# Kernel tuning notes

Hardware: AMD Instinct MI355X
Metric: run time of the kernel (lower is better)

The kernel has to match this reference:

```python
import jax, jax.numpy as jnp
import numpy as np

# canonical 3x3 lattice offsets, (dy,dx) pairs in row-major kernel order (mmcv offset layout)
CANON = jnp.array([[-1,-1],[-1,0],[-1,1],[0,-1],[0,0],[0,1],[1,-1],[1,0],[1,1]], dtype=jnp.float32)  # (9,2)
BASE_DILATION = 1.0

def conv3x3(x, w, b):
    # x: (B,Cin,H,W), w: (Cout,Cin,3,3), stride 1, pad 1
    y = jax.lax.conv_general_dilated(x, w, window_strides=(1, 1), padding=((1, 1), (1, 1)),
                                     dimension_numbers=('NCHW', 'OIHW', 'NCHW'))
    return y + b[None, :, None, None]

def _bilinear_sample(img, ys, xs):
    # img: (Cg,H,W); ys,xs: (9,H,W) float sample coords. Zero outside bounds (per-corner).
    Cg, Hn, Wn = img.shape
    y0 = jnp.floor(ys); x0 = jnp.floor(xs)
    wy = ys - y0; wx = xs - x0
    y0i = y0.astype(jnp.int32); x0i = x0.astype(jnp.int32)
    flat = img.reshape(Cg, Hn * Wn)
    def corner(yi, xi, w):
        valid = (yi >= 0) & (yi < Hn) & (xi >= 0) & (xi < Wn)
        idx = jnp.clip(yi, 0, Hn - 1) * Wn + jnp.clip(xi, 0, Wn - 1)
        v = jnp.take(flat, idx.reshape(-1), axis=1).reshape((Cg,) + yi.shape)
        return v * (w * valid.astype(img.dtype))[None]
    return (corner(y0i, x0i, (1 - wy) * (1 - wx)) + corner(y0i, x0i + 1, (1 - wy) * wx)
            + corner(y0i + 1, x0i, wy * (1 - wx)) + corner(y0i + 1, x0i + 1, wy * wx))  # (Cg,9,H,W)

def setup_inputs() -> dict:
    key = jax.random.key(0)
    ks = jax.random.split(key, 7)
    B, C, H, W = 4, 256, 64, 64
    O, dg = 256, 1
    x = jax.random.normal(ks[0], (B, C, H, W), dtype=jnp.float32)
    weight = jax.random.normal(ks[1], (O, C, 3, 3), dtype=jnp.float32) * (2.0 / (C * 9)) ** 0.5
    bias = jnp.zeros((O,), dtype=jnp.float32)
    w_scale = jax.random.normal(ks[2], (dg, C, 3, 3), dtype=jnp.float32) * 0.01
    b_scale = jnp.full((dg,), 0.5, dtype=jnp.float32)
    w_mask = jax.random.normal(ks[3], (dg * 9, C, 3, 3), dtype=jnp.float32) * 0.01
    b_mask = jnp.zeros((dg * 9,), dtype=jnp.float32)
    return {"x": x, "weight": weight, "bias": bias, "w_scale": w_scale,
            "b_scale": b_scale, "w_mask": w_mask, "b_mask": b_mask}

def reference(x, weight, bias, w_scale, b_scale, w_mask, b_mask):
    B, C, H, W = x.shape
    dg = w_scale.shape[0]
    O = weight.shape[0]
    Cg = C // dg
    # radial scale s(x) >= 0 (use_zero_dilation=False): (B,dg,H,W)
    scale = jax.nn.relu(conv3x3(x, w_scale, b_scale)) * BASE_DILATION
    # modulation mask: (B,dg,9,H,W)
    mask = jax.nn.sigmoid(conv3x3(x, w_mask, b_mask)).reshape(B, dg, 9, H, W)
    # learned offset = scale * canonical lattice: (B,dg,9,2,H,W)
    off = scale[:, :, None, None, :, :] * CANON[None, None, :, :, None, None]
    # sampling coords: p0 (out pos * stride - pad) + kernel offset * dilation(=1) + learned offset
    base_y = jnp.arange(H, dtype=x.dtype)[None, None, None, :, None] - 1.0  # pad=1
    base_x = jnp.arange(W, dtype=x.dtype)[None, None, None, None, :] - 1.0
    ys = base_y + CANON[:, 0][None, None, :, None, None] + off[:, :, :, 0]  # (B,dg,9,H,W)
    xs = base_x + CANON[:, 1][None, None, :, None, None] + off[:, :, :, 1]
    xg = x.reshape(B, dg, Cg, H, W)
    sampled = jax.vmap(jax.vmap(_bilinear_sample))(xg, ys, xs)  # (B,dg,Cg,9,H,W)
    val = (sampled * mask[:, :, None]).reshape(B, C, 9, H, W)
    out = jnp.einsum('bckhw,ock->bohw', val, weight.reshape(O, C, 9))
    return out + bias[None, :, None, None]
```

## Files before the change

### kernel.cpp

```cpp
#include <hip/hip_runtime.h>
#include <stdint.h>

#define B_ 4
#define C_ 256
#define H_ 64
#define W_ 64
#define O_ 256
#define K_ 2304
#define HW 4096
#define NPIX 16384

typedef unsigned short u16;
typedef __attribute__((ext_vector_type(8))) short bf16x8;
typedef __attribute__((ext_vector_type(4))) float f32x4;

__device__ __forceinline__ u16 f2bf(float f) {
    union { float f; uint32_t u; } v; v.f = f;
    uint32_t u = v.u;
    return (u16)((u + 0x7FFFu + ((u >> 16) & 1u)) >> 16);
}
__device__ __forceinline__ float bf2f(u16 u) {
    union { uint32_t u; float f; } v; v.u = ((uint32_t)u) << 16;
    return v.f;
}

__global__ __launch_bounds__(512) void k_scale_mask(
    const float* __restrict__ x, const float* __restrict__ w_scale,
    const float* __restrict__ w_mask, float* __restrict__ part)
{
    __shared__ float wsm[64 * 90];
    __shared__ float red[10 * 8 * 64];

    int bh = blockIdx.x;
    int cg = blockIdx.y;
    int b = bh >> 6, h = bh & 63;
    int tid = threadIdx.x;
    int w = tid & 63;
    int wv = tid >> 6;

    for (int i = tid; i < 64 * 90; i += 512) {
        int cl = i / 90, r = i % 90;
        int c = cg * 64 + cl;
        float v;
        if (r < 9) {
            v = w_scale[c * 9 + r];
        } else {
            int j = (r - 9) / 9, k = (r - 9) % 9;
            v = w_mask[((size_t)(j * C_ + c)) * 9 + k];
        }
        wsm[i] = v;
    }
    __syncthreads();

    float acc[10];
#pragma unroll
    for (int o = 0; o < 10; ++o) acc[o] = 0.f;

    const float* xb = x + (size_t)b * (C_ * HW);
#pragma unroll 1
    for (int cc = 0; cc < 8; ++cc) {
        int cl = wv * 8 + cc;
        const float* xp = xb + (cg * 64 + cl) * HW;
        float xv[9];
#pragma unroll
        for (int dy = -1; dy <= 1; ++dy) {
            int hh = h + dy;
            bool hv = (hh >= 0) && (hh < 64);
#pragma unroll
            for (int dx = -1; dx <= 1; ++dx) {
                int ww = w + dx;
                bool vld = hv && (ww >= 0) && (ww < 64);
                xv[(dy + 1) * 3 + (dx + 1)] = vld ? xp[hh * 64 + ww] : 0.f;
            }
        }
        const float* wrow = &wsm[cl * 90];
#pragma unroll
        for (int k = 0; k < 9; ++k) acc[0] = fmaf(xv[k], wrow[k], acc[0]);
#pragma unroll
        for (int j = 0; j < 9; ++j) {
#pragma unroll
            for (int k = 0; k < 9; ++k)
                acc[1 + j] = fmaf(xv[k], wrow[9 + j * 9 + k], acc[1 + j]);
        }
    }

#pragma unroll
    for (int o = 0; o < 10; ++o) red[(o * 8 + wv) * 64 + w] = acc[o];
    __syncthreads();
    if (tid < 64) {
        float* pout = part + ((size_t)(cg * 256 + bh) * 10) * 64 + tid;
#pragma unroll
        for (int o = 0; o < 10; ++o) {
            float t = 0.f;
#pragma unroll
            for (int g = 0; g < 8; ++g) t += red[(o * 8 + g) * 64 + tid];
            pout[o * 64] = t;
        }
    }
}

__global__ __launch_bounds__(256) void k_finalize(
    const float* __restrict__ part, const float* __restrict__ b_scale,
    const float* __restrict__ b_mask, float* __restrict__ scale_o,
    float* __restrict__ mask_o)
{
    int tid = threadIdx.x;
    int bh = blockIdx.x * 4 + (tid >> 6);
    int w = tid & 63;
    int b = bh >> 6, h = bh & 63;
#pragma unroll
    for (int o = 0; o < 10; ++o) {
        float t = 0.f;
#pragma unroll
        for (int cg = 0; cg < 4; ++cg)
            t += part[((size_t)(cg * 256 + bh) * 10 + o) * 64 + w];
        if (o == 0) {
            float s = t + b_scale[0];
            scale_o[bh * 64 + w] = s > 0.f ? s : 0.f;
        } else {
            float m = t + b_mask[o - 1];
            mask_o[(b * 9 + (o - 1)) * HW + h * 64 + w] = 1.f / (1.f + expf(-m));
        }
    }
}

__global__ __launch_bounds__(256) void k_pack_w(const float* __restrict__ wgt,
                                                u16* __restrict__ wbf)
{
    int k = blockIdx.x, o = blockIdx.y, c = threadIdx.x;
    wbf[(size_t)o * K_ + k * 256 + c] = f2bf(wgt[(size_t)o * K_ + c * 9 + k]);
}

__global__ __launch_bounds__(256) void k_transpose(const float* __restrict__ x,
                                                   u16* __restrict__ xT)
{
    __shared__ float t[64][65];
    int tid = threadIdx.x;
    int hw0 = blockIdx.x * 64, c0 = blockIdx.y * 64, b = blockIdx.z;

    {
        int hw4 = (tid & 15) * 4;
        int cr = tid >> 4;
        const float* xb = x + ((size_t)(b * 256 + c0)) * HW + hw0;
#pragma unroll
        for (int i = 0; i < 4; ++i) {
            int c = cr + i * 16;
            float4 v = *(const float4*)(xb + (size_t)c * HW + hw4);
            *(float4*)(&t[c][hw4]) = v;
        }
    }
    __syncthreads();
    {
        int c4 = (tid & 15) * 4;
        int hwr = tid >> 4;
        u16* xo = xT + ((size_t)(b * HW + hw0)) * 256 + c0;
#pragma unroll
        for (int i = 0; i < 4; ++i) {
            int hwl = hwr + i * 16;
            ushort4 o;
            o.x = f2bf(t[c4 + 0][hwl]);
            o.y = f2bf(t[c4 + 1][hwl]);
            o.z = f2bf(t[c4 + 2][hwl]);
            o.w = f2bf(t[c4 + 3][hwl]);
            *(ushort4*)(xo + (size_t)hwl * 256 + c4) = o;
        }
    }
}

__global__ __launch_bounds__(256) void k_val2(
    const u16* __restrict__ xT, const float* __restrict__ scale_i,
    const float* __restrict__ mask_i, u16* __restrict__ val)
{
    int wv = threadIdx.x >> 6, lane = threadIdx.x & 63;
    int p = blockIdx.x * 4 + wv;
    int b = p >> 12, hw = p & 4095;
    int h = hw >> 6, w = hw & 63;
    float d = 1.f + scale_i[p];
    const u16* xb = xT + ((size_t)(b << 12)) * 256;
    u16* vout = val + (size_t)p * K_;
    int c0 = lane * 4;

#pragma unroll 3
    for (int k = 0; k < 9; ++k) {
        int dy = k / 3 - 1, dx = k % 3 - 1;
        float ysf = (float)(h - 1) + (float)dy * d;
        float xsf = (float)(w - 1) + (float)dx * d;
        float y0f = floorf(ysf), x0f = floorf(xsf);
        float wy = ysf - y0f, wx = xsf - x0f;
        int y0 = (int)y0f, x0 = (int)x0f;
        int y1 = y0 + 1, x1 = x0 + 1;
        float vy0 = (y0 >= 0 && y0 < 64) ? 1.f : 0.f;
        float vy1 = (y1 >= 0 && y1 < 64) ? 1.f : 0.f;
        float vx0 = (x0 >= 0 && x0 < 64) ? 1.f : 0.f;
        float vx1 = (x1 >= 0 && x1 < 64) ? 1.f : 0.f;

        float m = mask_i[(b * 9 + k) * HW + hw];
        float w00 = (1.f - wy) * (1.f - wx) * m * vy0 * vx0;
        float w01 = (1.f - wy) * wx * m * vy0 * vx1;
        float w10 = wy * (1.f - wx) * m * vy1 * vx0;
        float w11 = wy * wx * m * vy1 * vx1;

        int cy0 = min(max(y0, 0), 63), cy1 = min(max(y1, 0), 63);
        int cx0 = min(max(x0, 0), 63), cx1 = min(max(x1, 0), 63);

        const u16* p00 = xb + (size_t)(cy0 * 64 + cx0) * 256 + c0;
        const u16* p01 = xb + (size_t)(cy0 * 64 + cx1) * 256 + c0;
        const u16* p10 = xb + (size_t)(cy1 * 64 + cx0) * 256 + c0;
        const u16* p11 = xb + (size_t)(cy1 * 64 + cx1) * 256 + c0;
        ushort4 v00 = *(const ushort4*)p00;
        ushort4 v01 = *(const ushort4*)p01;
        ushort4 v10 = *(const ushort4*)p10;
        ushort4 v11 = *(const ushort4*)p11;

        float rx = fmaf(w00, bf2f(v00.x), fmaf(w01, bf2f(v01.x), fmaf(w10, bf2f(v10.x), w11 * bf2f(v11.x))));
        float ry = fmaf(w00, bf2f(v00.y), fmaf(w01, bf2f(v01.y), fmaf(w10, bf2f(v10.y), w11 * bf2f(v11.y))));
        float rz = fmaf(w00, bf2f(v00.z), fmaf(w01, bf2f(v01.z), fmaf(w10, bf2f(v10.z), w11 * bf2f(v11.z))));
        float rw = fmaf(w00, bf2f(v00.w), fmaf(w01, bf2f(v01.w), fmaf(w10, bf2f(v10.w), w11 * bf2f(v11.w))));

        ushort4 pk;
        pk.x = f2bf(rx); pk.y = f2bf(ry); pk.z = f2bf(rz); pk.w = f2bf(rw);
        *(ushort4*)(vout + k * 256 + c0) = pk;
    }
}

__global__ __launch_bounds__(256, 2) void k_gemm(
    const u16* __restrict__ wbf, const u16* __restrict__ val,
    const float* __restrict__ bias, float* __restrict__ out)
{
    __shared__ u16 As[128 * 72];
    __shared__ u16 Bs[64 * 72];
    int tid = threadIdx.x;
    int lane = tid & 63;
    int wv = tid >> 6;
    int wm = wv >> 1, wn = wv & 1;
    int n0 = blockIdx.x * 64;
    int m0 = blockIdx.y * 128;
    int l15 = lane & 15, l4 = lane >> 4;

    f32x4 acc[4][2];
#pragma unroll
    for (int i = 0; i < 4; ++i)
#pragma unroll
        for (int j = 0; j < 2; ++j) acc[i][j] = (f32x4){0.f, 0.f, 0.f, 0.f};

    int rr = tid >> 3;
    int c8 = (tid & 7) * 8;

    for (int k0 = 0; k0 < K_; k0 += 64) {
        uint4 a0 = *(const uint4*)(wbf + (size_t)(m0 + rr) * K_ + k0 + c8);
        uint4 a1 = *(const uint4*)(wbf + (size_t)(m0 + rr + 32) * K_ + k0 + c8);
        uint4 a2 = *(const uint4*)(wbf + (size_t)(m0 + rr + 64) * K_ + k0 + c8);
        uint4 a3 = *(const uint4*)(wbf + (size_t)(m0 + rr + 96) * K_ + k0 + c8);
        uint4 b0 = *(const uint4*)(val + (size_t)(n0 + rr) * K_ + k0 + c8);
        uint4 b1 = *(const uint4*)(val + (size_t)(n0 + rr + 32) * K_ + k0 + c8);
        __syncthreads();
        *(uint4*)(As + rr * 72 + c8) = a0;
        *(uint4*)(As + (rr + 32) * 72 + c8) = a1;
        *(uint4*)(As + (rr + 64) * 72 + c8) = a2;
        *(uint4*)(As + (rr + 96) * 72 + c8) = a3;
        *(uint4*)(Bs + rr * 72 + c8) = b0;
        *(uint4*)(Bs + (rr + 32) * 72 + c8) = b1;
        __syncthreads();

#pragma unroll
        for (int kk = 0; kk < 2; ++kk) {
            bf16x8 af[4], bg[2];
#pragma unroll
            for (int i = 0; i < 4; ++i)
                af[i] = *(const bf16x8*)(As + (wm * 64 + i * 16 + l15) * 72 + kk * 32 + l4 * 8);
#pragma unroll
            for (int j = 0; j < 2; ++j)
                bg[j] = *(const bf16x8*)(Bs + (wn * 32 + j * 16 + l15) * 72 + kk * 32 + l4 * 8);
#pragma unroll
            for (int i = 0; i < 4; ++i)
#pragma unroll
                for (int j = 0; j < 2; ++j)
                    acc[i][j] = __builtin_amdgcn_mfma_f32_16x16x32_bf16(af[i], bg[j], acc[i][j], 0, 0, 0);
        }
    }

    int bidx = n0 >> 12;
    int hwbase = n0 & 4095;
#pragma unroll
    for (int i = 0; i < 4; ++i)
#pragma unroll
        for (int j = 0; j < 2; ++j)
#pragma unroll
            for (int t = 0; t < 4; ++t) {
                int row = wm * 64 + i * 16 + l4 * 4 + t;
                int col = wn * 32 + j * 16 + l15;
                int o = m0 + row;
                out[((size_t)(bidx * O_ + o)) * HW + hwbase + col] = acc[i][j][t] + bias[o];
            }
}

extern "C" void kernel_launch(void* const* d_in, const int* in_sizes, int n_in,
                              void* d_out, int out_size, void* d_ws, size_t ws_size,
                              hipStream_t stream) {
    const float* x       = (const float*)d_in[0];
    const float* weight  = (const float*)d_in[1];
    const float* bias    = (const float*)d_in[2];
    const float* w_scale = (const float*)d_in[3];
    const float* b_scale = (const float*)d_in[4];
    const float* w_mask  = (const float*)d_in[5];
    const float* b_mask  = (const float*)d_in[6];
    float* out = (float*)d_out;

    char* ws = (char*)d_ws;
    float* scale_ws = (float*)ws;
    float* mask_ws  = (float*)(ws + 65536);
    u16*   wbf      = (u16*)(ws + 65536 + 589824);
    u16*   val      = (u16*)(ws + 65536 + 589824 + 1179648);
    u16*   xT       = (u16*)(ws + 65536 + 589824 + 1179648 + 75497472);
    float* part_ws  = (float*)val;

    k_scale_mask<<<dim3(B_ * H_, 4), 512, 0, stream>>>(x, w_scale, w_mask, part_ws);
    k_finalize<<<dim3(64), 256, 0, stream>>>(part_ws, b_scale, b_mask, scale_ws, mask_ws);
    k_pack_w<<<dim3(9, O_), 256, 0, stream>>>(weight, wbf);
    k_transpose<<<dim3(HW / 64, C_ / 64, B_), 256, 0, stream>>>(x, xT);
    k_val2<<<dim3(NPIX / 4), 256, 0, stream>>>(xT, scale_ws, mask_ws, val);
    k_gemm<<<dim3(NPIX / 64, O_ / 128), 256, 0, stream>>>(wbf, val, bias, out);
}
```

Before: 175.4 us.

## Fuse bf16 NHWC transpose into scale/mask conv and prefetch GEMM tiles

The scale/mask conv kernel already loads every x value at the center tap. It now converts that value to bf16 and stages it in shared memory, then writes it out as the channel-last xT tile. This removes the separate transpose kernel launch and its extra read of x. The GEMM main loop also register-prefetches the next K tile's global loads while the current tile is being computed, which overlaps memory latency with MFMA work but costs more registers.

```diff
diff --git a/kernel.cpp b/kernel.cpp
--- a/kernel.cpp
+++ b/kernel.cpp
@@ -26,10 +26,12 @@
 
 __global__ __launch_bounds__(512) void k_scale_mask(
     const float* __restrict__ x, const float* __restrict__ w_scale,
-    const float* __restrict__ w_mask, float* __restrict__ part)
+    const float* __restrict__ w_mask, float* __restrict__ part,
+    u16* __restrict__ xT)
 {
     __shared__ float wsm[64 * 90];
     __shared__ float red[10 * 8 * 64];
+    __shared__ u16 xt[64 * 72];
 
     int bh = blockIdx.x;
     int cg = blockIdx.y;
@@ -73,6 +75,7 @@
                 xv[(dy + 1) * 3 + (dx + 1)] = vld ? xp[hh * 64 + ww] : 0.f;
             }
         }
+        xt[w * 72 + cl] = f2bf(xv[4]);
         const float* wrow = &wsm[cl * 90];
 #pragma unroll
         for (int k = 0; k < 9; ++k) acc[0] = fmaf(xv[k], wrow[k], acc[0]);
@@ -87,6 +90,13 @@
 #pragma unroll
     for (int o = 0; o < 10; ++o) red[(o * 8 + wv) * 64 + w] = acc[o];
     __syncthreads();
+
+    {
+        int ww = tid >> 3, c8 = (tid & 7) * 8;
+        uint4 v = *(const uint4*)(xt + ww * 72 + c8);
+        *(uint4*)(xT + ((size_t)(bh * 64 + ww)) * 256 + cg * 64 + c8) = v;
+    }
+
     if (tid < 64) {
         float* pout = part + ((size_t)(cg * 256 + bh) * 10) * 64 + tid;
 #pragma unroll
@@ -129,42 +139,6 @@
 {
     int k = blockIdx.x, o = blockIdx.y, c = threadIdx.x;
     wbf[(size_t)o * K_ + k * 256 + c] = f2bf(wgt[(size_t)o * K_ + c * 9 + k]);
-}
-
-__global__ __launch_bounds__(256) void k_transpose(const float* __restrict__ x,
-                                                   u16* __restrict__ xT)
-{
-    __shared__ float t[64][65];
-    int tid = threadIdx.x;
-    int hw0 = blockIdx.x * 64, c0 = blockIdx.y * 64, b = blockIdx.z;
-
-    {
-        int hw4 = (tid & 15) * 4;
-        int cr = tid >> 4;
-        const float* xb = x + ((size_t)(b * 256 + c0)) * HW + hw0;
-#pragma unroll
-        for (int i = 0; i < 4; ++i) {
-            int c = cr + i * 16;
-            float4 v = *(const float4*)(xb + (size_t)c * HW + hw4);
-            *(float4*)(&t[c][hw4]) = v;
-        }
-    }
-    __syncthreads();
-    {
-        int c4 = (tid & 15) * 4;
-        int hwr = tid >> 4;
-        u16* xo = xT + ((size_t)(b * HW + hw0)) * 256 + c0;
-#pragma unroll
-        for (int i = 0; i < 4; ++i) {
-            int hwl = hwr + i * 16;
-            ushort4 o;
-            o.x = f2bf(t[c4 + 0][hwl]);
-            o.y = f2bf(t[c4 + 1][hwl]);
-            o.z = f2bf(t[c4 + 2][hwl]);
-            o.w = f2bf(t[c4 + 3][hwl]);
-            *(ushort4*)(xo + (size_t)hwl * 256 + c4) = o;
-        }
-    }
 }
 
 __global__ __launch_bounds__(256) void k_val2(
@@ -246,21 +220,35 @@
     int rr = tid >> 3;
     int c8 = (tid & 7) * 8;
 
+    const u16* ap = wbf + (size_t)(m0 + rr) * K_ + c8;
+    const u16* bp = val + (size_t)(n0 + rr) * K_ + c8;
+
+    uint4 ra0 = *(const uint4*)(ap);
+    uint4 ra1 = *(const uint4*)(ap + (size_t)32 * K_);
+    uint4 ra2 = *(const uint4*)(ap + (size_t)64 * K_);
+    uint4 ra3 = *(const uint4*)(ap + (size_t)96 * K_);
+    uint4 rb0 = *(const uint4*)(bp);
+    uint4 rb1 = *(const uint4*)(bp + (size_t)32 * K_);
+
     for (int k0 = 0; k0 < K_; k0 += 64) {
-        uint4 a0 = *(const uint4*)(wbf + (size_t)(m0 + rr) * K_ + k0 + c8);
-        uint4 a1 = *(const uint4*)(wbf + (size_t)(m0 + rr + 32) * K_ + k0 + c8);
-        uint4 a2 = *(const uint4*)(wbf + (size_t)(m0 + rr + 64) * K_ + k0 + c8);
-        uint4 a3 = *(const uint4*)(wbf + (size_t)(m0 + rr + 96) * K_ + k0 + c8);
-        uint4 b0 = *(const uint4*)(val + (size_t)(n0 + rr) * K_ + k0 + c8);
-        uint4 b1 = *(const uint4*)(val + (size_t)(n0 + rr + 32) * K_ + k0 + c8);
         __syncthreads();
-        *(uint4*)(As + rr * 72 + c8) = a0;
-        *(uint4*)(As + (rr + 32) * 72 + c8) = a1;
-        *(uint4*)(As + (rr + 64) * 72 + c8) = a2;
-        *(uint4*)(As + (rr + 96) * 72 + c8) = a3;
-        *(uint4*)(Bs + rr * 72 + c8) = b0;
-        *(uint4*)(Bs + (rr + 32) * 72 + c8) = b1;
+        *(uint4*)(As + rr * 72 + c8) = ra0;
+        *(uint4*)(As + (rr + 32) * 72 + c8) = ra1;
+        *(uint4*)(As + (rr + 64) * 72 + c8) = ra2;
+        *(uint4*)(As + (rr + 96) * 72 + c8) = ra3;
+        *(uint4*)(Bs + rr * 72 + c8) = rb0;
+        *(uint4*)(Bs + (rr + 32) * 72 + c8) = rb1;
         __syncthreads();
+
+        int kn = k0 + 64;
+        if (kn < K_) {
+            ra0 = *(const uint4*)(ap + kn);
+            ra1 = *(const uint4*)(ap + (size_t)32 * K_ + kn);
+            ra2 = *(const uint4*)(ap + (size_t)64 * K_ + kn);
+            ra3 = *(const uint4*)(ap + (size_t)96 * K_ + kn);
+            rb0 = *(const uint4*)(bp + kn);
+            rb1 = *(const uint4*)(bp + (size_t)32 * K_ + kn);
+        }
 
 #pragma unroll
         for (int kk = 0; kk < 2; ++kk) {
@@ -314,10 +302,9 @@
     u16*   xT       = (u16*)(ws + 65536 + 589824 + 1179648 + 75497472);
     float* part_ws  = (float*)val;
 
-    k_scale_mask<<<dim3(B_ * H_, 4), 512, 0, stream>>>(x, w_scale, w_mask, part_ws);
+    k_scale_mask<<<dim3(B_ * H_, 4), 512, 0, stream>>>(x, w_scale, w_mask, part_ws, xT);
     k_finalize<<<dim3(64), 256, 0, stream>>>(part_ws, b_scale, b_mask, scale_ws, mask_ws);
     k_pack_w<<<dim3(9, O_), 256, 0, stream>>>(weight, wbf);
-    k_transpose<<<dim3(HW / 64, C_ / 64, B_), 256, 0, stream>>>(x, xT);
     k_val2<<<dim3(NPIX / 4), 256, 0, stream>>>(xT, scale_ws, mask_ws, val);
     k_gemm<<<dim3(NPIX / 64, O_ / 128), 256, 0, stream>>>(wbf, val, bias, out);
 }
```

Measured after the change: 174.4 us. No clear change (-0.6%).
